# Performance work log

Measured on AMD Instinct MI355X. Metric: run time of the kernel, lower is better.

The kernel has to match this reference:

```python
import jax, jax.numpy as jnp
import numpy as np

N_NODES = 100_000
N_EDGES = 1_600_000
N_FEAT = 11
HIDDEN = 128
N_GRAPHS = 4096


def gcn_conv(x, W, b, row, col, n_nodes):
    # PyG GCNConv (default): add self-loops, symmetric deg^-1/2 norm,
    # out[col] += norm * (x @ W)[row], then + bias.
    xw = x @ W  # [N, H]
    ew = jnp.ones(row.shape[0], dtype=xw.dtype)
    deg = jax.ops.segment_sum(ew, col, num_segments=n_nodes)
    dis = jnp.where(deg > 0, jax.lax.rsqrt(deg), 0.0).astype(xw.dtype)
    norm = dis[row] * dis[col]  # [E+N]
    msg = xw[row] * norm[:, None]  # gather + scale
    out = jax.ops.segment_sum(msg, col, num_segments=n_nodes)  # scatter-add
    return out + b


def setup_inputs() -> dict:
    key = jax.random.key(0)
    ks = jax.random.split(key, 12)
    x = jax.random.normal(ks[0], (N_NODES, N_FEAT), dtype=jnp.float32)
    edge_index = jax.random.randint(ks[1], (2, N_EDGES), 0, N_NODES, dtype=jnp.int64)
    batch = jnp.sort(jax.random.randint(ks[2], (N_NODES,), 0, N_GRAPHS, dtype=jnp.int64))

    def glorot(k, shape):
        lim = float(np.sqrt(6.0 / (shape[0] + shape[1])))
        return jax.random.uniform(k, shape, jnp.float32, -lim, lim)

    W1 = glorot(ks[3], (N_FEAT, HIDDEN))
    b1 = jnp.zeros((HIDDEN,), jnp.float32)
    W2 = glorot(ks[4], (HIDDEN, HIDDEN))
    b2 = jnp.zeros((HIDDEN,), jnp.float32)
    Wl1 = glorot(ks[5], (HIDDEN, HIDDEN))
    bl1 = jnp.zeros((HIDDEN,), jnp.float32)
    Wl2 = glorot(ks[6], (HIDDEN, 1))
    bl2 = jnp.zeros((1,), jnp.float32)
    return {"x": x, "W1": W1, "b1": b1, "W2": W2, "b2": b2,
            "Wl1": Wl1, "bl1": bl1, "Wl2": Wl2, "bl2": bl2,
            "edge_index": edge_index, "batch": batch}


def reference(x, W1, b1, W2, b2, Wl1, bl1, Wl2, bl2, edge_index, batch):
    n = x.shape[0]
    loops = jnp.arange(n, dtype=edge_index.dtype)
    row = jnp.concatenate([edge_index[0], loops])
    col = jnp.concatenate([edge_index[1], loops])

    h = jax.nn.relu(gcn_conv(x, W1, b1, row, col, n))
    h = jax.nn.relu(gcn_conv(h, W2, b2, row, col, n))

    # global_mean_pool over per-node graph ids
    sums = jax.ops.segment_sum(h, batch, num_segments=N_GRAPHS)
    cnts = jax.ops.segment_sum(jnp.ones((n,), h.dtype), batch, num_segments=N_GRAPHS)
    pooled = sums / jnp.maximum(cnts, 1.0)[:, None]  # [G, H]

    out = jax.nn.relu(pooled @ Wl1 + bl1) @ Wl2 + bl2  # [G, 1]
    return out
```

## Files before the change

kernel.cpp:

```cpp
#include <hip/hip_runtime.h>

#define NN 100000
#define NE 1600000
#define NF 11
#define HID 128
#define NG 4096
#define NB 391

#define BSH 7
#define BNODES 128
#define NBK 782
#define CAP 3072
#define EPB 4096
#define NBB 391

typedef short bf16x8 __attribute__((ext_vector_type(8)));
typedef float f32x4 __attribute__((ext_vector_type(4)));

__device__ __forceinline__ unsigned short f2bf(float f) {
    unsigned u = __float_as_uint(f);
    return (unsigned short)((u + 0x7FFFu + ((u >> 16) & 1u)) >> 16);
}
__device__ __forceinline__ unsigned packbf(float a, float b) {
    return (unsigned)f2bf(a) | ((unsigned)f2bf(b) << 16);
}
__device__ __forceinline__ float bflo(unsigned v) { return __uint_as_float(v << 16); }
__device__ __forceinline__ float bfhi(unsigned v) { return __uint_as_float(v & 0xFFFF0000u); }
__device__ __forceinline__ bf16x8 as_bf(uint4 u) { union { uint4 a; bf16x8 b; } v; v.a = u; return v.b; }

__global__ void k_zero(int* __restrict__ p, int n) {
    int i = blockIdx.x * blockDim.x + threadIdx.x;
    if (i < n) p[i] = 0;
}

__global__ __launch_bounds__(256) void k_bucket(const int* __restrict__ row, const int* __restrict__ col,
                                                int* __restrict__ bcur, int* __restrict__ staging) {
    __shared__ int cnt[NBK];
    __shared__ int loc[NBK];
    const int tid = threadIdx.x;
    const int e0 = blockIdx.x * EPB;
    for (int i = tid; i < NBK; i += 256) { cnt[i] = 0; loc[i] = 0; }
    __syncthreads();
    int rb[16]; unsigned pay[16];
#pragma unroll
    for (int j = 0; j < 16; ++j) {
        int e = e0 + j * 256 + tid;
        int c = (e < NE) ? col[e] : -1;
        int r = (e < NE) ? row[e] : 0;
        rb[j] = (c >= 0) ? (c >> BSH) : -1;
        pay[j] = (unsigned)r | ((unsigned)(c & (BNODES - 1)) << 17);
        if (rb[j] >= 0) atomicAdd(&cnt[rb[j]], 1);
    }
    __syncthreads();
    for (int b = tid; b < NBK; b += 256) {
        int c = cnt[b];
        cnt[b] = (c > 0) ? atomicAdd(&bcur[b], c) : 0;
    }
    __syncthreads();
#pragma unroll
    for (int j = 0; j < 16; ++j) {
        if (rb[j] >= 0) {
            int p = cnt[rb[j]] + atomicAdd(&loc[rb[j]], 1);
            staging[rb[j] * CAP + p] = (int)pay[j];
        }
    }
}

__global__ __launch_bounds__(256) void k_hist2(const int* __restrict__ staging, const int* __restrict__ bcur,
                                               int* __restrict__ degE, float* __restrict__ dis) {
    __shared__ int cnt[BNODES];
    const int b = blockIdx.x, tid = threadIdx.x;
    if (tid < BNODES) cnt[tid] = 0;
    __syncthreads();
    const int sz = bcur[b];
    const int base = b * CAP;
    for (int i = tid; i < sz; i += 256)
        atomicAdd(&cnt[((unsigned)staging[base + i]) >> 17], 1);
    __syncthreads();
    int n = b * BNODES + tid;
    if (tid < BNODES && n < NN) {
        int d = cnt[tid];
        degE[n] = d;
        dis[n] = rsqrtf((float)(d + 1));
    }
}

__global__ void k_scan1(const int* __restrict__ degE, int* __restrict__ startp, int* __restrict__ partial) {
    __shared__ int sh[256];
    int t = threadIdx.x, i = blockIdx.x * 256 + t;
    int v = (i < NN) ? degE[i] : 0;
    sh[t] = v; __syncthreads();
    for (int off = 1; off < 256; off <<= 1) {
        int u = (t >= off) ? sh[t - off] : 0; __syncthreads();
        sh[t] += u; __syncthreads();
    }
    if (i < NN) startp[i] = sh[t] - v;
    if (t == 255) partial[blockIdx.x] = sh[255];
}

__global__ void k_scan2(int* __restrict__ partial) {
    __shared__ int sh[512];
    int t = threadIdx.x;
    int v = (t < NB) ? partial[t] : 0;
    sh[t] = v; __syncthreads();
    for (int off = 1; off < 512; off <<= 1) {
        int u = (t >= off) ? sh[t - off] : 0; __syncthreads();
        sh[t] += u; __syncthreads();
    }
    if (t < NB) partial[t] = sh[t] - v;
}

__global__ void k_scan3(int* __restrict__ startp, const int* __restrict__ partial) {
    int i = blockIdx.x * 256 + threadIdx.x;
    if (i < NN) startp[i] += partial[blockIdx.x];
    if (i == 0) startp[NN] = NE;
}

__global__ __launch_bounds__(256) void k_fillb(const int* __restrict__ staging, const int* __restrict__ bcur,
                                               const int* __restrict__ startp, int* __restrict__ csr) {
    __shared__ int cur[BNODES];
    const int b = blockIdx.x, tid = threadIdx.x;
    int n = b * BNODES + tid;
    if (tid < BNODES) cur[tid] = (n < NN) ? startp[n] : 0;
    __syncthreads();
    const int sz = bcur[b];
    const int base = b * CAP;
    for (int i = tid; i < sz; i += 256) {
        unsigned p = (unsigned)staging[base + i];
        int pos = atomicAdd(&cur[p >> 17], 1);
        csr[pos] = (int)(p & 0x1FFFF);
    }
}

__global__ void k_w2t(const float* __restrict__ W2, unsigned* __restrict__ w2t) {
    int i = blockIdx.x * 256 + threadIdx.x;
    if (i >= HID * 64) return;
    int col = i >> 6, kw = i & 63;
    w2t[col * 64 + kw] = packbf(W2[(2 * kw) * HID + col], W2[(2 * kw + 1) * HID + col]);
}

__global__ __launch_bounds__(256) void k_xd(const float* __restrict__ x, const float* __restrict__ dis,
                                            unsigned* __restrict__ xd8) {
    const int n = blockIdx.x * 16 + (threadIdx.x >> 4);
    const int lane = threadIdx.x & 15;
    float f = (lane < NF) ? x[(size_t)n * NF + lane] : 0.f;
    f *= dis[n];
    float g = __shfl_down(f, 1, 16);
    if ((lane & 1) == 0 && lane < NF)
        xd8[n * 8 + (lane >> 1)] = packbf(f, g);
}

__global__ __launch_bounds__(256) void k_gat1(const unsigned* __restrict__ xd8,
                                              const int* __restrict__ startp,
                                              const int* __restrict__ csr,
                                              float2* __restrict__ aggf2) {
    const int node = blockIdx.x * 4 + (threadIdx.x >> 6);
    const int lane = threadIdx.x & 63;
    const int g = lane >> 3, f = lane & 7;
    const int s = startp[node], e = startp[node + 1];
    float ax = 0.f, ay = 0.f;
    for (int i = s; i < e; i += 64) {
        int idx = (i + lane < e) ? csr[i + lane] : 0;
        int m = e - i;
#pragma unroll
        for (int t = 0; t < 8; ++t) {
            if (t * 8 >= m) break;
            int ei2 = t * 8 + g;
            int r = __shfl(idx, ei2);
            unsigned v = (ei2 < m && f < 6) ? xd8[r * 8 + f] : 0u;
            ax += bflo(v); ay += bfhi(v);
        }
    }
    ax += __shfl_xor(ax, 8);  ay += __shfl_xor(ay, 8);
    ax += __shfl_xor(ax, 16); ay += __shfl_xor(ay, 16);
    ax += __shfl_xor(ax, 32); ay += __shfl_xor(ay, 32);
    if (g == 0 && f < 6) {
        unsigned sv = xd8[node * 8 + f];
        aggf2[node * 8 + f] = make_float2(ax + bflo(sv), ay + bfhi(sv));
    }
}

__global__ __launch_bounds__(256) void k_l1l2(const float2* __restrict__ aggf2,
                                              const float* __restrict__ W1,
                                              const float* __restrict__ b1,
                                              const unsigned* __restrict__ w2t,
                                              const float* __restrict__ dis,
                                              unsigned* __restrict__ yb) {
    __shared__ float w1s[NF * HID];
    __shared__ float xs[64 * 16];
    __shared__ unsigned h1s[64 * 64];
    const int tid = threadIdx.x;
    const int n0 = blockIdx.x * 64;
    const int wid = tid >> 6, lane = tid & 63;
    const int lr = lane & 15, lk = lane >> 4;
    const int colb = wid * 32;

    for (int i = tid; i < NF * HID; i += 256) w1s[i] = W1[i];
#pragma unroll
    for (int p = 0; p < 2; ++p) {
        int idx = p * 256 + tid;
        int nl = idx >> 3, l = idx & 7;
        int n = n0 + nl;
        float2 v = make_float2(0.f, 0.f);
        if (l < 6 && n < NN) v = aggf2[(size_t)n * 8 + l];
        xs[nl * 16 + 2 * l] = v.x;
        xs[nl * 16 + 2 * l + 1] = v.y;
    }
    const uint4* w4 = (const uint4*)w2t;
    bf16x8 Bf[2][4];
#pragma unroll
    for (int c = 0; c < 2; ++c)
#pragma unroll
        for (int ks = 0; ks < 4; ++ks)
            Bf[c][ks] = as_bf(w4[(colb + c * 16 + lr) * 16 + ks * 4 + lk]);
    __syncthreads();

    const int f2 = tid & 63, sub = tid >> 6;
    float2 bb = ((const float2*)b1)[f2];
    const int jsw = f2 >> 2, ci = f2 & 3;
#pragma unroll
    for (int p = 0; p < 16; ++p) {
        int nl = p * 4 + sub;
        int n = n0 + nl;
        float s0 = 0.f, s1 = 0.f;
#pragma unroll
        for (int k = 0; k < NF; ++k) {
            float xv = xs[nl * 16 + k];
            s0 = fmaf(xv, w1s[k * HID + f2 * 2], s0);
            s1 = fmaf(xv, w1s[k * HID + f2 * 2 + 1], s1);
        }
        float d = (n < NN) ? dis[n] : 0.f;
        float ax = fmaxf(fmaf(s0, d, bb.x), 0.f);
        float ay = fmaxf(fmaf(s1, d, bb.y), 0.f);
        h1s[nl * 64 + ((jsw ^ (nl & 15)) << 2) + ci] = packbf(ax, ay);
    }
    __syncthreads();

    const uint4* h4 = (const uint4*)h1s;
    f32x4 acc[4][2];
#pragma unroll
    for (int r = 0; r < 4; ++r)
#pragma unroll
        for (int c = 0; c < 2; ++c) {
            f32x4 z = {0.f, 0.f, 0.f, 0.f};
            acc[r][c] = z;
        }
#pragma unroll
    for (int ks = 0; ks < 4; ++ks) {
        bf16x8 Af[4];
#pragma unroll
        for (int r = 0; r < 4; ++r)
            Af[r] = as_bf(h4[(r * 16 + lr) * 16 + ((ks * 4 + lk) ^ lr)]);
#pragma unroll
        for (int r = 0; r < 4; ++r)
#pragma unroll
            for (int c = 0; c < 2; ++c)
                acc[r][c] = __builtin_amdgcn_mfma_f32_16x16x32_bf16(Af[r], Bf[c][ks], acc[r][c], 0, 0, 0);
    }

#pragma unroll
    for (int r = 0; r < 4; ++r) {
#pragma unroll
        for (int i = 0; i < 4; ++i) {
            int nd = n0 + r * 16 + lk * 4 + i;
            float d = (nd < NN) ? dis[nd] : 0.f;
#pragma unroll
            for (int c = 0; c < 2; ++c) {
                float v = acc[r][c][i] * d;
                float o = __shfl_xor(v, 1);
                if (!(lane & 1) && nd < NN) {
                    int col = colb + c * 16 + lr;
                    yb[nd * 64 + (col >> 1)] = packbf(v, o);
                }
            }
        }
    }
}

__global__ __launch_bounds__(256) void k_gather(const unsigned* __restrict__ yb,
                                                const int* __restrict__ startp,
                                                const int* __restrict__ csr_rows,
                                                const float* __restrict__ dis,
                                                const float* __restrict__ b,
                                                unsigned* __restrict__ hb) {
    const int node = blockIdx.x * 4 + (threadIdx.x >> 6);
    const int lane = threadIdx.x & 63;
    int s = startp[node], e = startp[node + 1];
    unsigned sv = yb[node * 64 + lane];
    float ax = bflo(sv), ay = bfhi(sv);
    for (int i = s; i < e; i += 64) {
        int idx = (i + lane < e) ? csr_rows[i + lane] : 0;
        int m = min(64, e - i);
        int j = 0;
        for (; j + 15 < m; j += 16) {
            unsigned v[16];
#pragma unroll
            for (int u = 0; u < 16; ++u) {
                int r = __shfl(idx, j + u);
                v[u] = yb[r * 64 + lane];
            }
#pragma unroll
            for (int u = 0; u < 16; ++u) { ax += bflo(v[u]); ay += bfhi(v[u]); }
        }
        for (; j + 7 < m; j += 8) {
            unsigned v[8];
#pragma unroll
            for (int u = 0; u < 8; ++u) {
                int r = __shfl(idx, j + u);
                v[u] = yb[r * 64 + lane];
            }
#pragma unroll
            for (int u = 0; u < 8; ++u) { ax += bflo(v[u]); ay += bfhi(v[u]); }
        }
        for (; j + 3 < m; j += 4) {
            unsigned v[4];
#pragma unroll
            for (int u = 0; u < 4; ++u) {
                int r = __shfl(idx, j + u);
                v[u] = yb[r * 64 + lane];
            }
#pragma unroll
            for (int u = 0; u < 4; ++u) { ax += bflo(v[u]); ay += bfhi(v[u]); }
        }
        for (; j < m; ++j) {
            int r = __shfl(idx, j);
            unsigned v = yb[r * 64 + lane];
            ax += bflo(v); ay += bfhi(v);
        }
    }
    float d = dis[node];
    float2 bb = ((const float2*)b)[lane];
    ax = fmaxf(fmaf(ax, d, bb.x), 0.f);
    ay = fmaxf(fmaf(ay, d, bb.y), 0.f);
    hb[node * 64 + lane] = packbf(ax, ay);
}

__global__ void k_bounds(const int* __restrict__ batch, int* __restrict__ gs) {
    int g = blockIdx.x * blockDim.x + threadIdx.x;
    if (g > NG) return;
    int lo = 0, hi = NN;
    while (lo < hi) {
        int mid = (lo + hi) >> 1;
        if (batch[mid] < g) lo = mid + 1; else hi = mid;
    }
    gs[g] = lo;
}

__global__ __launch_bounds__(64) void k_pool(const unsigned* __restrict__ hb, const int* __restrict__ gs,
                                             float* __restrict__ pooled) {
    int g = blockIdx.x, f2 = threadIdx.x;
    int s = gs[g], e = gs[g + 1];
    float ax = 0.f, ay = 0.f;
    for (int n = s; n < e; ++n) {
        unsigned v = hb[(size_t)n * 64 + f2];
        ax += bflo(v); ay += bfhi(v);
    }
    float inv = 1.0f / (float)max(e - s, 1);
    pooled[(size_t)g * HID + f2 * 2] = ax * inv;
    pooled[(size_t)g * HID + f2 * 2 + 1] = ay * inv;
}

__global__ __launch_bounds__(128) void k_head(const float* __restrict__ pooled,
                                              const float* __restrict__ Wl1, const float* __restrict__ bl1,
                                              const float* __restrict__ Wl2, const float* __restrict__ bl2,
                                              float* __restrict__ out) {
    __shared__ float p[HID];
    __shared__ float red[128];
    const int g = blockIdx.x, f = threadIdx.x;
    p[f] = pooled[(size_t)g * HID + f];
    __syncthreads();
    float s = bl1[f];
    for (int k = 0; k < HID; ++k) s = fmaf(p[k], Wl1[k * HID + f], s);
    s = fmaxf(s, 0.f);
    red[f] = s * Wl2[f];
    __syncthreads();
    for (int off = 64; off > 0; off >>= 1) {
        if (f < off) red[f] += red[f + off];
        __syncthreads();
    }
    if (f == 0) out[g] = red[0] + bl2[0];
}

extern "C" void kernel_launch(void* const* d_in, const int* in_sizes, int n_in,
                              void* d_out, int out_size, void* d_ws, size_t ws_size,
                              hipStream_t stream) {
    const float* x   = (const float*)d_in[0];
    const float* W1  = (const float*)d_in[1];
    const float* b1  = (const float*)d_in[2];
    const float* W2  = (const float*)d_in[3];
    const float* b2  = (const float*)d_in[4];
    const float* Wl1 = (const float*)d_in[5];
    const float* bl1 = (const float*)d_in[6];
    const float* Wl2 = (const float*)d_in[7];
    const float* bl2 = (const float*)d_in[8];
    const int* ei    = (const int*)d_in[9];
    const int* batch = (const int*)d_in[10];
    float* out = (float*)d_out;

    const int* row = ei;
    const int* col = ei + NE;

    char* ws = (char*)d_ws;
    size_t off = 0;
    unsigned* yb   = (unsigned*)(ws + off); off += (size_t)NN * 64 * 4;
    unsigned* hb   = (unsigned*)(ws + off); off += (size_t)NN * 64 * 4;
    unsigned* xd8  = (unsigned*)(ws + off); off += (size_t)NN * 8 * 4;
    float2* aggf2  = (float2*)  (ws + off); off += (size_t)NN * 8 * 8;
    int*   degE    = (int*)  (ws + off); off += (size_t)NN * 4;
    float* dis     = (float*)(ws + off); off += (size_t)NN * 4;
    int*   startp  = (int*)  (ws + off); off += (size_t)(NN + 1) * 4;
    int*   partial = (int*)  (ws + off); off += 512 * 4;
    int*   csr     = (int*)  (ws + off); off += (size_t)NE * 4;
    int*   gs      = (int*)  (ws + off); off += (size_t)(NG + 1) * 4;
    float* pooled  = (float*)(ws + off); off += (size_t)NG * HID * 4;
    int*   bcur    = (int*)  (ws + off); off += (size_t)NBK * 4;
    unsigned* w2t  = (unsigned*)(ws + off); off += (size_t)HID * 64 * 4;
    int*   staging = (int*)hb;

    k_zero<<<(NBK + 255) / 256, 256, 0, stream>>>(bcur, NBK);
    k_bucket<<<NBB, 256, 0, stream>>>(row, col, bcur, staging);
    k_hist2<<<NBK, 256, 0, stream>>>(staging, bcur, degE, dis);
    k_scan1<<<NB, 256, 0, stream>>>(degE, startp, partial);
    k_scan2<<<1, 512, 0, stream>>>(partial);
    k_scan3<<<NB, 256, 0, stream>>>(startp, partial);
    k_fillb<<<NBK, 256, 0, stream>>>(staging, bcur, startp, csr);
    k_bounds<<<(NG + 256) / 256, 256, 0, stream>>>(batch, gs);
    k_w2t<<<(HID * 64 + 255) / 256, 256, 0, stream>>>(W2, w2t);

    k_xd<<<NN / 16, 256, 0, stream>>>(x, dis, xd8);
    k_gat1<<<NN / 4, 256, 0, stream>>>(xd8, startp, csr, aggf2);
    k_l1l2<<<(NN + 63) / 64, 256, 0, stream>>>(aggf2, W1, b1, w2t, dis, yb);

    k_gather<<<NN / 4, 256, 0, stream>>>(yb, startp, csr, dis, b2, hb);

    k_pool<<<NG, 64, 0, stream>>>(hb, gs, pooled);
    k_head<<<NG, 128, 0, stream>>>(pooled, Wl1, bl1, Wl2, bl2, out);
}
```

Before: 220.3 us.

## Fuse preprocessing kernels, stage l1l2 output via LDS, restructure pool and head

Merges the zero, W2-transpose and graph-bounds kernels into one launch. The degree histogram now does the per-bucket scan itself, so the CSR fill applies the bucket offsets and the separate scan passes go away. The l1l2 epilogue writes its tile to a swizzled shared-memory buffer first and then stores to global as coalesced 16-byte vectors. Pooling splits nodes across 4 waves, the head caches Wl1 in LDS for 16 graphs per block, and the 16-way unrolled gather path is removed. The aim is fewer launches and better memory coalescing, at the cost of more LDS use and some extra syncs.

Measured after the change: 206.2 us. -6.4%, faster.

```diff
diff --git a/kernel.cpp b/kernel.cpp
--- a/kernel.cpp
+++ b/kernel.cpp
@@ -5,7 +5,6 @@
 #define NF 11
 #define HID 128
 #define NG 4096
-#define NB 391
 
 #define BSH 7
 #define BNODES 128
@@ -28,9 +27,25 @@
 __device__ __forceinline__ float bfhi(unsigned v) { return __uint_as_float(v & 0xFFFF0000u); }
 __device__ __forceinline__ bf16x8 as_bf(uint4 u) { union { uint4 a; bf16x8 b; } v; v.a = u; return v.b; }
 
-__global__ void k_zero(int* __restrict__ p, int n) {
-    int i = blockIdx.x * blockDim.x + threadIdx.x;
-    if (i < n) p[i] = 0;
+__global__ __launch_bounds__(256) void k_misc(int* __restrict__ bcur,
+                                              const float* __restrict__ W2, unsigned* __restrict__ w2t,
+                                              const int* __restrict__ batch, int* __restrict__ gs,
+                                              int* __restrict__ startp) {
+    int i = blockIdx.x * 256 + threadIdx.x;
+    if (i < NBK) bcur[i] = 0;
+    if (i < HID * 64) {
+        int col = i >> 6, kw = i & 63;
+        w2t[col * 64 + kw] = packbf(W2[(2 * kw) * HID + col], W2[(2 * kw + 1) * HID + col]);
+    }
+    if (i <= NG) {
+        int lo = 0, hi = NN;
+        while (lo < hi) {
+            int mid = (lo + hi) >> 1;
+            if (batch[mid] < i) lo = mid + 1; else hi = mid;
+        }
+        gs[i] = lo;
+    }
+    if (i == 0) startp[NN] = NE;
 }
 
 __global__ __launch_bounds__(256) void k_bucket(const int* __restrict__ row, const int* __restrict__ col,
@@ -66,9 +81,11 @@
     }
 }
 
-__global__ __launch_bounds__(256) void k_hist2(const int* __restrict__ staging, const int* __restrict__ bcur,
-                                               int* __restrict__ degE, float* __restrict__ dis) {
+__global__ __launch_bounds__(256) void k_hist2s(const int* __restrict__ staging, const int* __restrict__ bcur,
+                                                float* __restrict__ dis, int* __restrict__ startp,
+                                                int* __restrict__ partial) {
     __shared__ int cnt[BNODES];
+    __shared__ int sc[BNODES];
     const int b = blockIdx.x, tid = threadIdx.x;
     if (tid < BNODES) cnt[tid] = 0;
     __syncthreads();
@@ -77,51 +94,50 @@
     for (int i = tid; i < sz; i += 256)
         atomicAdd(&cnt[((unsigned)staging[base + i]) >> 17], 1);
     __syncthreads();
+    int v = (tid < BNODES) ? cnt[tid] : 0;
+    if (tid < BNODES) sc[tid] = v;
+    __syncthreads();
+    for (int off = 1; off < BNODES; off <<= 1) {
+        int u = (tid < BNODES && tid >= off) ? sc[tid - off] : 0;
+        __syncthreads();
+        if (tid < BNODES) sc[tid] += u;
+        __syncthreads();
+    }
     int n = b * BNODES + tid;
     if (tid < BNODES && n < NN) {
-        int d = cnt[tid];
-        degE[n] = d;
-        dis[n] = rsqrtf((float)(d + 1));
-    }
-}
-
-__global__ void k_scan1(const int* __restrict__ degE, int* __restrict__ startp, int* __restrict__ partial) {
-    __shared__ int sh[256];
-    int t = threadIdx.x, i = blockIdx.x * 256 + t;
-    int v = (i < NN) ? degE[i] : 0;
+        startp[n] = sc[tid] - v;
+        dis[n] = rsqrtf((float)(v + 1));
+    }
+    if (tid == BNODES - 1) partial[b] = sc[BNODES - 1];
+}
+
+__global__ __launch_bounds__(1024) void k_scan2(int* __restrict__ partial) {
+    __shared__ int sh[1024];
+    int t = threadIdx.x;
+    int v = (t < NBK) ? partial[t] : 0;
     sh[t] = v; __syncthreads();
-    for (int off = 1; off < 256; off <<= 1) {
+    for (int off = 1; off < 1024; off <<= 1) {
         int u = (t >= off) ? sh[t - off] : 0; __syncthreads();
         sh[t] += u; __syncthreads();
     }
-    if (i < NN) startp[i] = sh[t] - v;
-    if (t == 255) partial[blockIdx.x] = sh[255];
-}
-
-__global__ void k_scan2(int* __restrict__ partial) {
-    __shared__ int sh[512];
-    int t = threadIdx.x;
-    int v = (t < NB) ? partial[t] : 0;
-    sh[t] = v; __syncthreads();
-    for (int off = 1; off < 512; off <<= 1) {
-        int u = (t >= off) ? sh[t - off] : 0; __syncthreads();
-        sh[t] += u; __syncthreads();
-    }
-    if (t < NB) partial[t] = sh[t] - v;
-}
-
-__global__ void k_scan3(int* __restrict__ startp, const int* __restrict__ partial) {
-    int i = blockIdx.x * 256 + threadIdx.x;
-    if (i < NN) startp[i] += partial[blockIdx.x];
-    if (i == 0) startp[NN] = NE;
-}
-
-__global__ __launch_bounds__(256) void k_fillb(const int* __restrict__ staging, const int* __restrict__ bcur,
-                                               const int* __restrict__ startp, int* __restrict__ csr) {
+    if (t < NBK) partial[t] = sh[t] - v;
+}
+
+__global__ __launch_bounds__(256) void k_fillbs(const int* __restrict__ staging, const int* __restrict__ bcur,
+                                                const int* __restrict__ partial,
+                                                int* __restrict__ startp, int* __restrict__ csr) {
     __shared__ int cur[BNODES];
     const int b = blockIdx.x, tid = threadIdx.x;
+    const int bb = partial[b];
     int n = b * BNODES + tid;
-    if (tid < BNODES) cur[tid] = (n < NN) ? startp[n] : 0;
+    if (tid < BNODES) {
+        int sfin = 0;
+        if (n < NN) {
+            sfin = startp[n] + bb;
+            startp[n] = sfin;
+        }
+        cur[tid] = sfin;
+    }
     __syncthreads();
     const int sz = bcur[b];
     const int base = b * CAP;
@@ -130,13 +146,6 @@
         int pos = atomicAdd(&cur[p >> 17], 1);
         csr[pos] = (int)(p & 0x1FFFF);
     }
-}
-
-__global__ void k_w2t(const float* __restrict__ W2, unsigned* __restrict__ w2t) {
-    int i = blockIdx.x * 256 + threadIdx.x;
-    if (i >= HID * 64) return;
-    int col = i >> 6, kw = i & 63;
-    w2t[col * 64 + kw] = packbf(W2[(2 * kw) * HID + col], W2[(2 * kw + 1) * HID + col]);
 }
 
 __global__ __launch_bounds__(256) void k_xd(const float* __restrict__ x, const float* __restrict__ dis,
@@ -257,23 +266,38 @@
             for (int c = 0; c < 2; ++c)
                 acc[r][c] = __builtin_amdgcn_mfma_f32_16x16x32_bf16(Af[r], Bf[c][ks], acc[r][c], 0, 0, 0);
     }
+    __syncthreads();
 
 #pragma unroll
     for (int r = 0; r < 4; ++r) {
 #pragma unroll
         for (int i = 0; i < 4; ++i) {
-            int nd = n0 + r * 16 + lk * 4 + i;
+            int ndl = r * 16 + lk * 4 + i;
+            int nd = n0 + ndl;
             float d = (nd < NN) ? dis[nd] : 0.f;
+            int swz = ((r * 4 + lk) & 3) << 3;
 #pragma unroll
             for (int c = 0; c < 2; ++c) {
                 float v = acc[r][c][i] * d;
                 float o = __shfl_xor(v, 1);
-                if (!(lane & 1) && nd < NN) {
-                    int col = colb + c * 16 + lr;
-                    yb[nd * 64 + (col >> 1)] = packbf(v, o);
+                if (!(lane & 1)) {
+                    int cu = (colb >> 1) + c * 8 + (lr >> 1);
+                    h1s[ndl * 64 + (cu ^ swz)] = packbf(v, o);
                 }
             }
         }
+    }
+    __syncthreads();
+    uint4* yb4 = (uint4*)yb;
+    const uint4* h1s4 = (const uint4*)h1s;
+#pragma unroll
+    for (int it = 0; it < 4; ++it) {
+        int idx4 = it * 256 + tid;
+        int ndl = idx4 >> 4, cu4 = (idx4 & 15) * 4;
+        int s = (ndl >> 2) & 3;
+        int nd = n0 + ndl;
+        if (nd < NN)
+            yb4[(size_t)nd * 16 + (idx4 & 15)] = h1s4[(ndl * 64 + (cu4 ^ (s << 3))) >> 2];
     }
 }
 
@@ -292,16 +316,6 @@
         int idx = (i + lane < e) ? csr_rows[i + lane] : 0;
         int m = min(64, e - i);
         int j = 0;
-        for (; j + 15 < m; j += 16) {
-            unsigned v[16];
-#pragma unroll
-            for (int u = 0; u < 16; ++u) {
-                int r = __shfl(idx, j + u);
-                v[u] = yb[r * 64 + lane];
-            }
-#pragma unroll
-            for (int u = 0; u < 16; ++u) { ax += bflo(v[u]); ay += bfhi(v[u]); }
-        }
         for (; j + 7 < m; j += 8) {
             unsigned v[8];
 #pragma unroll
@@ -335,50 +349,58 @@
     hb[node * 64 + lane] = packbf(ax, ay);
 }
 
-__global__ void k_bounds(const int* __restrict__ batch, int* __restrict__ gs) {
-    int g = blockIdx.x * blockDim.x + threadIdx.x;
-    if (g > NG) return;
-    int lo = 0, hi = NN;
-    while (lo < hi) {
-        int mid = (lo + hi) >> 1;
-        if (batch[mid] < g) lo = mid + 1; else hi = mid;
-    }
-    gs[g] = lo;
-}
-
-__global__ __launch_bounds__(64) void k_pool(const unsigned* __restrict__ hb, const int* __restrict__ gs,
-                                             float* __restrict__ pooled) {
-    int g = blockIdx.x, f2 = threadIdx.x;
+__global__ __launch_bounds__(256) void k_pool(const unsigned* __restrict__ hb, const int* __restrict__ gs,
+                                              float* __restrict__ pooled) {
+    __shared__ float rx[4][64], ry[4][64];
+    const int g = blockIdx.x;
+    const int w = threadIdx.x >> 6, lane = threadIdx.x & 63;
     int s = gs[g], e = gs[g + 1];
     float ax = 0.f, ay = 0.f;
-    for (int n = s; n < e; ++n) {
-        unsigned v = hb[(size_t)n * 64 + f2];
+    for (int n = s + w; n < e; n += 4) {
+        unsigned v = hb[(size_t)n * 64 + lane];
         ax += bflo(v); ay += bfhi(v);
     }
-    float inv = 1.0f / (float)max(e - s, 1);
-    pooled[(size_t)g * HID + f2 * 2] = ax * inv;
-    pooled[(size_t)g * HID + f2 * 2 + 1] = ay * inv;
-}
-
-__global__ __launch_bounds__(128) void k_head(const float* __restrict__ pooled,
+    rx[w][lane] = ax; ry[w][lane] = ay;
+    __syncthreads();
+    if (w == 0) {
+        ax = rx[0][lane] + rx[1][lane] + rx[2][lane] + rx[3][lane];
+        ay = ry[0][lane] + ry[1][lane] + ry[2][lane] + ry[3][lane];
+        float inv = 1.0f / (float)max(e - s, 1);
+        pooled[(size_t)g * HID + lane * 2] = ax * inv;
+        pooled[(size_t)g * HID + lane * 2 + 1] = ay * inv;
+    }
+}
+
+__global__ __launch_bounds__(256) void k_head(const float* __restrict__ pooled,
                                               const float* __restrict__ Wl1, const float* __restrict__ bl1,
                                               const float* __restrict__ Wl2, const float* __restrict__ bl2,
                                               float* __restrict__ out) {
-    __shared__ float p[HID];
-    __shared__ float red[128];
-    const int g = blockIdx.x, f = threadIdx.x;
-    p[f] = pooled[(size_t)g * HID + f];
-    __syncthreads();
-    float s = bl1[f];
-    for (int k = 0; k < HID; ++k) s = fmaf(p[k], Wl1[k * HID + f], s);
-    s = fmaxf(s, 0.f);
-    red[f] = s * Wl2[f];
-    __syncthreads();
-    for (int off = 64; off > 0; off >>= 1) {
-        if (f < off) red[f] += red[f + off];
+    __shared__ float wl[HID * HID];
+    __shared__ float p[2][HID];
+    __shared__ float red[4];
+    const int tid = threadIdx.x;
+    const int f = tid & 127, half = tid >> 7;
+    const int w = tid >> 6, lane = tid & 63;
+    for (int i = tid; i < HID * HID; i += 256) wl[i] = Wl1[i];
+    const float w2f = Wl2[f];
+    const float b1f = bl1[f];
+    const float b2f = bl2[0];
+    const int g0 = blockIdx.x * 16;
+    for (int gi = 0; gi < 16; gi += 2) {
+        int g = g0 + gi + half;
+        p[half][f] = pooled[(size_t)g * HID + f];
         __syncthreads();
-    }
-    if (f == 0) out[g] = red[0] + bl2[0];
+        float s = b1f;
+#pragma unroll 16
+        for (int k = 0; k < HID; ++k) s = fmaf(p[half][k], wl[k * HID + f], s);
+        s = fmaxf(s, 0.f) * w2f;
+#pragma unroll
+        for (int off = 1; off < 64; off <<= 1) s += __shfl_xor(s, off);
+        if (lane == 0) red[w] = s;
+        __syncthreads();
+        if (tid < 2) out[g0 + gi + tid] = red[tid * 2] + red[tid * 2 + 1] + b2f;
+        __syncthreads();
+    }
 }
 
 extern "C" void kernel_launch(void* const* d_in, const int* in_sizes, int n_in,
@@ -406,10 +428,9 @@
     unsigned* hb   = (unsigned*)(ws + off); off += (size_t)NN * 64 * 4;
     unsigned* xd8  = (unsigned*)(ws + off); off += (size_t)NN * 8 * 4;
     float2* aggf2  = (float2*)  (ws + off); off += (size_t)NN * 8 * 8;
-    int*   degE    = (int*)  (ws + off); off += (size_t)NN * 4;
     float* dis     = (float*)(ws + off); off += (size_t)NN * 4;
     int*   startp  = (int*)  (ws + off); off += (size_t)(NN + 1) * 4;
-    int*   partial = (int*)  (ws + off); off += 512 * 4;
+    int*   partial = (int*)  (ws + off); off += 1024 * 4;
     int*   csr     = (int*)  (ws + off); off += (size_t)NE * 4;
     int*   gs      = (int*)  (ws + off); off += (size_t)(NG + 1) * 4;
     float* pooled  = (float*)(ws + off); off += (size_t)NG * HID * 4;
@@ -417,15 +438,11 @@
     unsigned* w2t  = (unsigned*)(ws + off); off += (size_t)HID * 64 * 4;
     int*   staging = (int*)hb;
 
-    k_zero<<<(NBK + 255) / 256, 256, 0, stream>>>(bcur, NBK);
+    k_misc<<<32, 256, 0, stream>>>(bcur, W2, w2t, batch, gs, startp);
     k_bucket<<<NBB, 256, 0, stream>>>(row, col, bcur, staging);
-    k_hist2<<<NBK, 256, 0, stream>>>(staging, bcur, degE, dis);
-    k_scan1<<<NB, 256, 0, stream>>>(degE, startp, partial);
-    k_scan2<<<1, 512, 0, stream>>>(partial);
-    k_scan3<<<NB, 256, 0, stream>>>(startp, partial);
-    k_fillb<<<NBK, 256, 0, stream>>>(staging, bcur, startp, csr);
-    k_bounds<<<(NG + 256) / 256, 256, 0, stream>>>(batch, gs);
-    k_w2t<<<(HID * 64 + 255) / 256, 256, 0, stream>>>(W2, w2t);
+    k_hist2s<<<NBK, 256, 0, stream>>>(staging, bcur, dis, startp, partial);
+    k_scan2<<<1, 1024, 0, stream>>>(partial);
+    k_fillbs<<<NBK, 256, 0, stream>>>(staging, bcur, partial, startp, csr);
 
     k_xd<<<NN / 16, 256, 0, stream>>>(x, dis, xd8);
     k_gat1<<<NN / 4, 256, 0, stream>>>(xd8, startp, csr, aggf2);
@@ -433,6 +450,6 @@
 
     k_gather<<<NN / 4, 256, 0, stream>>>(yb, startp, csr, dis, b2, hb);
 
-    k_pool<<<NG, 64, 0, stream>>>(hb, gs, pooled);
-    k_head<<<NG, 128, 0, stream>>>(pooled, Wl1, bl1, Wl2, bl2, out);
-}
+    k_pool<<<NG, 256, 0, stream>>>(hb, gs, pooled);
+    k_head<<<NG / 16, 256, 0, stream>>>(pooled, Wl1, bl1, Wl2, bl2, out);
+}
```
